# Optimization experiments

Measured on AMD Instinct MI355X. Metric: run time of the kernel, lower is better.

Reference implementation:

```python
import jax, jax.numpy as jnp
import numpy as np

T, B, S, V, D = 64, 32, 400, 32000, 1536  # timesteps, batch, post len, vocab, dh+2*eh


def setup_inputs() -> dict:
    key = jax.random.key(0)
    k0, k1, k2, k3, k4 = jax.random.split(key, 5)
    return {
        "h": jax.random.normal(k0, (T, B, D), jnp.float32),
        "W": jax.random.normal(k1, (D, V), jnp.float32) * 0.02,
        "b": jnp.zeros((V,), jnp.float32),
        # attention weights over post positions (rows sum to 1, like the model's softmax attention)
        "att": jax.nn.softmax(jax.random.normal(k2, (T, B, S), jnp.float32), axis=-1),
        # generation probability in (0,1)
        "p_gen": jax.nn.sigmoid(jax.random.normal(k3, (T, B, 1), jnp.float32)),
        # post token ids, seq-first (S, B) as in the original data layout
        "post": jax.random.randint(k4, (S, B), 0, V),
    }


def reference(h, W, b, att, p_gen, post):
    # gen.w = wLinearLayer(gen.h): (T,B,D) @ (D,V) + (V,)
    w = jnp.einsum('tbd,dv->tbv', h, W) + b
    # sum_on_voc_index: scatter-add att[t,b,s] into voc_att[t,b,post[s,b]].
    # (The torch code builds a dense (B,V,S) zero buffer, scatter_'s the same
    # positions every timestep and sums over S -- identical to this scatter-add.)
    idx = post.T                                   # (B, S)
    b_idx = jnp.arange(B)[:, None]                 # (B, 1) -> broadcasts with idx
    voc_att = jnp.zeros((T, B, V), w.dtype).at[:, b_idx, idx].add(att)
    # pointer-generator mixture
    return p_gen * w + (1.0 - p_gen) * voc_att
```

## Files before the change

### kernel.cpp

```cpp
#include <hip/hip_runtime.h>
#include <hip/hip_bf16.h>
#include <stdint.h>

#define T_DIM 64
#define B_DIM 32
#define S_DIM 400
#define V_DIM 32000
#define D_DIM 1536
#define M_DIM (T_DIM * B_DIM)

typedef __attribute__((ext_vector_type(8))) short bf16x8;
typedef __attribute__((ext_vector_type(4))) float f32x4;


static __device__ __forceinline__ unsigned short f2bf(float x) {
    union { float f; uint32_t u; } v; v.f = x;
    uint32_t r = (v.u + 0x7FFFu + ((v.u >> 16) & 1u)) >> 16;
    return (unsigned short)r;
}

static __device__ __forceinline__ void gload_lds16(const void* g, void* l) {
    __builtin_amdgcn_global_load_lds(
        (const __attribute__((address_space(1))) uint32_t*)g,
        (__attribute__((address_space(3))) uint32_t*)l,
        16, 0, 0);
}


__global__ void convert_h(const float* __restrict__ h, unsigned short* __restrict__ hb) {
    const size_t n4 = (size_t)M_DIM * D_DIM / 4;
    for (size_t i = (size_t)blockIdx.x * blockDim.x + threadIdx.x; i < n4;
         i += (size_t)gridDim.x * blockDim.x) {
        const float4 v = ((const float4*)h)[i];
        ushort4 o;
        o.x = f2bf(v.x); o.y = f2bf(v.y); o.z = f2bf(v.z); o.w = f2bf(v.w);
        ((ushort4*)hb)[i] = o;
    }
}


__global__ __launch_bounds__(256)
void convT_W(const float* __restrict__ W, unsigned short* __restrict__ Wt) {
    __shared__ unsigned short lds[64 * 66];
    const int k0 = blockIdx.x * 64;
    const int v0 = blockIdx.y * 64;
    const int tid = threadIdx.x;
    const int rr = tid >> 4;
    const int cc = (tid & 15) * 4;

    #pragma unroll
    for (int p = 0; p < 4; ++p) {
        const int r = p * 16 + rr;
        const float4 v = *(const float4*)&W[(size_t)(k0 + r) * V_DIM + v0 + cc];
        unsigned short* q = &lds[r * 66 + cc];
        q[0] = f2bf(v.x); q[1] = f2bf(v.y); q[2] = f2bf(v.z); q[3] = f2bf(v.w);
    }
    __syncthreads();
    #pragma unroll
    for (int p = 0; p < 4; ++p) {
        const int n = p * 16 + rr;
        ushort4 o;
        o.x = lds[(cc + 0) * 66 + n];
        o.y = lds[(cc + 1) * 66 + n];
        o.z = lds[(cc + 2) * 66 + n];
        o.w = lds[(cc + 3) * 66 + n];
        *(ushort4*)&Wt[(size_t)(v0 + n) * D_DIM + k0 + cc] = o;
    }
}


#define BM 128
#define BN 128
#define BK 32
#define NKT (D_DIM / BK)

__global__ __launch_bounds__(256, 2)
void gemm_mfma(const unsigned short* __restrict__ A,
               const unsigned short* __restrict__ Bt,
               const float* __restrict__ bias,
               const float* __restrict__ p_gen,
               float* __restrict__ out) {
    __shared__ unsigned short lds[2][2][BM * BK];

    const int bid = blockIdx.x;
    const int mt = bid & 15;
    const int nt = bid >> 4;
    const int m0 = mt * BM;
    const int n0 = nt * BN;
    const int tid = threadIdx.x;
    const int lane = tid & 63;
    const int wid = tid >> 6;
    const int wr = wid >> 1;
    const int wc = wid & 1;

    f32x4 acc[4][4] = {};

    auto stage = [&](int buf, int kt) {
        const int k0 = kt * BK;
        #pragma unroll
        for (int i = 0; i < 2; ++i) {
            const int o = tid * 16 + i * 4096;
            const int row = o >> 6;
            const int colb = o & 63;
            const char* ga = (const char*)A + ((size_t)(m0 + row) * D_DIM + k0) * 2 + colb;
            gload_lds16(ga, (char*)&lds[buf][0][0] + o);
            const char* gb = (const char*)Bt + ((size_t)(n0 + row) * D_DIM + k0) * 2 + colb;
            gload_lds16(gb, (char*)&lds[buf][1][0] + o);
        }
    };

    const int kq = (lane >> 4) * 8;
    const int rq = lane & 15;

    auto compute = [&](int buf) {
        const unsigned short* As = &lds[buf][0][0];
        const unsigned short* Bs = &lds[buf][1][0];
        bf16x8 a[4], b[4];
        #pragma unroll
        for (int i = 0; i < 4; ++i) {
            a[i] = *(const bf16x8*)&As[(wr * 64 + i * 16 + rq) * BK + kq];
            b[i] = *(const bf16x8*)&Bs[(wc * 64 + i * 16 + rq) * BK + kq];
        }
        #pragma unroll
        for (int mi = 0; mi < 4; ++mi)
            #pragma unroll
            for (int ni = 0; ni < 4; ++ni)
                acc[mi][ni] = __builtin_amdgcn_mfma_f32_16x16x32_bf16(a[mi], b[ni], acc[mi][ni], 0, 0, 0);
    };

    stage(0, 0);
    int cur = 0;
    for (int kt = 0; kt < NKT; ++kt) {
        __syncthreads();
        if (kt + 1 < NKT) stage(cur ^ 1, kt + 1);
        compute(cur);
        cur ^= 1;
    }

    const int rr4 = (lane >> 4) * 4;
    #pragma unroll
    for (int mi = 0; mi < 4; ++mi) {
        #pragma unroll
        for (int r = 0; r < 4; ++r) {
            const int m = m0 + wr * 64 + mi * 16 + rr4 + r;
            const float pg = p_gen[m];
            #pragma unroll
            for (int ni = 0; ni < 4; ++ni) {
                const int n = n0 + wc * 64 + ni * 16 + rq;
                out[(size_t)m * V_DIM + n] = pg * (acc[mi][ni][r] + bias[n]);
            }
        }
    }
}


__global__ void scatter_att(const float* __restrict__ att, const float* __restrict__ p_gen,
                            const int* __restrict__ post, float* __restrict__ out) {
    const int tb = blockIdx.x;
    const int b = tb & (B_DIM - 1);
    const float g = 1.0f - p_gen[tb];
    float* o = out + (size_t)tb * V_DIM;
    const float* a = att + (size_t)tb * S_DIM;
    for (int s = threadIdx.x; s < S_DIM; s += blockDim.x) {
        atomicAdd(&o[post[s * B_DIM + b]], g * a[s]);
    }
}


#define FB_MT 16
__global__ __launch_bounds__(256)
void gemm_naive(const float* __restrict__ h, const float* __restrict__ W,
                const float* __restrict__ bias, const float* __restrict__ pg,
                float* __restrict__ out) {
    const int mb = blockIdx.y;
    const int v = blockIdx.x * 256 + threadIdx.x;
    __shared__ float hs[FB_MT][128];
    float acc[FB_MT] = {};
    for (int k0 = 0; k0 < D_DIM; k0 += 128) {
        for (int i = threadIdx.x; i < FB_MT * 128; i += 256)
            hs[i >> 7][i & 127] = h[(size_t)(mb * FB_MT + (i >> 7)) * D_DIM + k0 + (i & 127)];
        __syncthreads();
        for (int kk = 0; kk < 128; ++kk) {
            const float wv = W[(size_t)(k0 + kk) * V_DIM + v];
            #pragma unroll
            for (int i = 0; i < FB_MT; ++i) acc[i] += hs[i][kk] * wv;
        }
        __syncthreads();
    }
    #pragma unroll
    for (int i = 0; i < FB_MT; ++i) {
        const int m = mb * FB_MT + i;
        out[(size_t)m * V_DIM + v] = pg[m] * (acc[i] + bias[v]);
    }
}


extern "C" void kernel_launch(void* const* d_in, const int* in_sizes, int n_in,
                              void* d_out, int out_size, void* d_ws, size_t ws_size,
                              hipStream_t stream) {
    const float* h    = (const float*)d_in[0];
    const float* W    = (const float*)d_in[1];
    const float* bias = (const float*)d_in[2];
    const float* att  = (const float*)d_in[3];
    const float* pg   = (const float*)d_in[4];
    const int*   post = (const int*)d_in[5];
    float* out = (float*)d_out;

    const size_t wt_bytes = (size_t)V_DIM * D_DIM * 2;
    const size_t hb_bytes = (size_t)M_DIM * D_DIM * 2;

    if (ws_size >= wt_bytes + hb_bytes) {
        unsigned short* Wt = (unsigned short*)d_ws;
        unsigned short* hb = (unsigned short*)((char*)d_ws + wt_bytes);
        convert_h<<<1024, 256, 0, stream>>>(h, hb);
        dim3 tg(D_DIM / 64, V_DIM / 64);
        convT_W<<<tg, 256, 0, stream>>>(W, Wt);
        gemm_mfma<<<16 * 250, 256, 0, stream>>>(hb, Wt, bias, pg, out);
    } else {
        dim3 fg(V_DIM / 256, M_DIM / FB_MT);
        gemm_naive<<<fg, 256, 0, stream>>>(h, W, bias, pg, out);
    }

    scatter_att<<<M_DIM, 256, 0, stream>>>(att, pg, post, out);
}
```

Before: 389.6 us.

## Replace 128x128 GEMM with 256x256-tile 4-stage pipelined MFMA kernel

Replaces the bf16 MFMA GEMM with a 512-thread kernel that computes 256x256 output tiles. It uses a 4-buffer LDS ring with loads issued three k-steps ahead and tracked by explicit vmcnt waits. An XOR swizzle on LDS addresses is meant to avoid bank conflicts, a block-index swizzle is meant to improve L2 reuse of W tiles, and s_setprio is raised around the MFMA bursts. The larger tiles cut global and LDS traffic per FLOP, at the cost of about 128KB of LDS per block, so residency is likely one block per CU, plus more barriers per k-step.

```diff
diff --git a/kernel.cpp b/kernel.cpp
--- a/kernel.cpp
+++ b/kernel.cpp
@@ -11,6 +11,9 @@
 
 typedef __attribute__((ext_vector_type(8))) short bf16x8;
 typedef __attribute__((ext_vector_type(4))) float f32x4;
+
+#define MEMFENCE asm volatile("" ::: "memory")
+#define BARRIER() do { MEMFENCE; __builtin_amdgcn_s_barrier(); MEMFENCE; } while (0)
 
 
 static __device__ __forceinline__ unsigned short f2bf(float x) {
@@ -69,88 +72,124 @@
 }
 
 
-#define BM 128
-#define BN 128
-#define BK 32
-#define NKT (D_DIM / BK)
-
-__global__ __launch_bounds__(256, 2)
-void gemm_mfma(const unsigned short* __restrict__ A,
-               const unsigned short* __restrict__ Bt,
-               const float* __restrict__ bias,
-               const float* __restrict__ p_gen,
-               float* __restrict__ out) {
-    __shared__ unsigned short lds[2][2][BM * BK];
+#define GBM 256
+#define GBN 256
+#define GBK 32
+#define GNKT (D_DIM / GBK)
+
+__global__ __launch_bounds__(512, 2)
+void gemm_mfma256(const unsigned short* __restrict__ A,
+                  const unsigned short* __restrict__ Bt,
+                  const float* __restrict__ bias,
+                  const float* __restrict__ p_gen,
+                  float* __restrict__ out) {
+    __shared__ unsigned short ldsA[4][GBM * GBK];
+    __shared__ unsigned short ldsB[4][GBN * GBK];
 
     const int bid = blockIdx.x;
-    const int mt = bid & 15;
-    const int nt = bid >> 4;
-    const int m0 = mt * BM;
-    const int n0 = nt * BN;
+    const int swz = (bid & 7) * 125 + (bid >> 3);
+    const int m0 = (swz & 7) * GBM;
+    const int n0 = (swz >> 3) * GBN;
+
     const int tid = threadIdx.x;
     const int lane = tid & 63;
     const int wid = tid >> 6;
-    const int wr = wid >> 1;
-    const int wc = wid & 1;
-
-    f32x4 acc[4][4] = {};
-
-    auto stage = [&](int buf, int kt) {
-        const int k0 = kt * BK;
-        #pragma unroll
-        for (int i = 0; i < 2; ++i) {
-            const int o = tid * 16 + i * 4096;
-            const int row = o >> 6;
-            const int colb = o & 63;
-            const char* ga = (const char*)A + ((size_t)(m0 + row) * D_DIM + k0) * 2 + colb;
-            gload_lds16(ga, (char*)&lds[buf][0][0] + o);
-            const char* gb = (const char*)Bt + ((size_t)(n0 + row) * D_DIM + k0) * 2 + colb;
-            gload_lds16(gb, (char*)&lds[buf][1][0] + o);
-        }
-    };
-
+    const int wr = wid >> 2;
+    const int wc = wid & 3;
+    const int rq = lane & 15;
     const int kq = (lane >> 4) * 8;
-    const int rq = lane & 15;
-
-    auto compute = [&](int buf) {
-        const unsigned short* As = &lds[buf][0][0];
-        const unsigned short* Bs = &lds[buf][1][0];
+
+    const char* gA[2]; const char* gB[2]; int ldsOff[2];
+    #pragma unroll
+    for (int j = 0; j < 2; ++j) {
+        const int o = tid * 16 + j * 8192;
+        const int row = o >> 6;
+        const int lc = (o & 63) ^ (((row >> 1) & 3) << 4);
+        gA[j] = (const char*)A + (size_t)(m0 + row) * D_DIM * 2 + lc;
+        gB[j] = (const char*)Bt + (size_t)(n0 + row) * D_DIM * 2 + lc;
+        ldsOff[j] = o;
+    }
+
+    #define STAGE2(kt, j)                                                        \
+        do {                                                                     \
+            const int _b = (kt) & 3;                                             \
+            gload_lds16(gA[j] + (size_t)(kt) * (GBK * 2),                        \
+                        (char*)&ldsA[_b][0] + ldsOff[j]);                        \
+            gload_lds16(gB[j] + (size_t)(kt) * (GBK * 2),                        \
+                        (char*)&ldsB[_b][0] + ldsOff[j]);                        \
+        } while (0)
+
+    int aOff0[4], aOff1[4], bOff[4];
+    #pragma unroll
+    for (int i = 0; i < 4; ++i) {
+        int r0 = wr * 128 + i * 16 + rq;
+        int r1 = r0 + 64;
+        aOff0[i] = r0 * 64 + ((kq * 2) ^ (((r0 >> 1) & 3) << 4));
+        aOff1[i] = r1 * 64 + ((kq * 2) ^ (((r1 >> 1) & 3) << 4));
+        int rb = wc * 64 + i * 16 + rq;
+        bOff[i] = rb * 64 + ((kq * 2) ^ (((rb >> 1) & 3) << 4));
+    }
+
+    f32x4 acc[8][4] = {};
+
+    #pragma unroll
+    for (int t = 0; t < 3; ++t) { STAGE2(t, 0); STAGE2(t, 1); }
+    asm volatile("s_waitcnt vmcnt(8)" ::: "memory");
+    BARRIER();
+
+    for (int kt = 0; kt < GNKT; ++kt) {
+        const char* As = (const char*)&ldsA[kt & 3][0];
+        const char* Bs = (const char*)&ldsB[kt & 3][0];
         bf16x8 a[4], b[4];
-        #pragma unroll
-        for (int i = 0; i < 4; ++i) {
-            a[i] = *(const bf16x8*)&As[(wr * 64 + i * 16 + rq) * BK + kq];
-            b[i] = *(const bf16x8*)&Bs[(wc * 64 + i * 16 + rq) * BK + kq];
-        }
+
+        #pragma unroll
+        for (int i = 0; i < 4; ++i) a[i] = *(const bf16x8*)(As + aOff0[i]);
+        #pragma unroll
+        for (int j = 0; j < 4; ++j) b[j] = *(const bf16x8*)(Bs + bOff[j]);
+        if (kt + 3 < GNKT) STAGE2(kt + 3, 0);
+        BARRIER();
+        __builtin_amdgcn_s_setprio(1);
         #pragma unroll
         for (int mi = 0; mi < 4; ++mi)
             #pragma unroll
-            for (int ni = 0; ni < 4; ++ni)
-                acc[mi][ni] = __builtin_amdgcn_mfma_f32_16x16x32_bf16(a[mi], b[ni], acc[mi][ni], 0, 0, 0);
-    };
-
-    stage(0, 0);
-    int cur = 0;
-    for (int kt = 0; kt < NKT; ++kt) {
-        __syncthreads();
-        if (kt + 1 < NKT) stage(cur ^ 1, kt + 1);
-        compute(cur);
-        cur ^= 1;
+            for (int nj = 0; nj < 4; ++nj)
+                acc[mi][nj] = __builtin_amdgcn_mfma_f32_16x16x32_bf16(a[mi], b[nj], acc[mi][nj], 0, 0, 0);
+        __builtin_amdgcn_s_setprio(0);
+        BARRIER();
+
+        #pragma unroll
+        for (int i = 0; i < 4; ++i) a[i] = *(const bf16x8*)(As + aOff1[i]);
+        if (kt + 3 < GNKT) STAGE2(kt + 3, 1);
+        BARRIER();
+        __builtin_amdgcn_s_setprio(1);
+        #pragma unroll
+        for (int mi = 0; mi < 4; ++mi)
+            #pragma unroll
+            for (int nj = 0; nj < 4; ++nj)
+                acc[4 + mi][nj] = __builtin_amdgcn_mfma_f32_16x16x32_bf16(a[mi], b[nj], acc[4 + mi][nj], 0, 0, 0);
+        __builtin_amdgcn_s_setprio(0);
+
+        if (kt < GNKT - 3)       { asm volatile("s_waitcnt vmcnt(8)" ::: "memory"); }
+        else if (kt == GNKT - 3) { asm volatile("s_waitcnt vmcnt(4)" ::: "memory"); }
+        else if (kt == GNKT - 2) { asm volatile("s_waitcnt vmcnt(0)" ::: "memory"); }
+        BARRIER();
     }
 
     const int rr4 = (lane >> 4) * 4;
     #pragma unroll
-    for (int mi = 0; mi < 4; ++mi) {
+    for (int mi = 0; mi < 8; ++mi) {
         #pragma unroll
         for (int r = 0; r < 4; ++r) {
-            const int m = m0 + wr * 64 + mi * 16 + rr4 + r;
-            const float pg = p_gen[m];
-            #pragma unroll
-            for (int ni = 0; ni < 4; ++ni) {
-                const int n = n0 + wc * 64 + ni * 16 + rq;
-                out[(size_t)m * V_DIM + n] = pg * (acc[mi][ni][r] + bias[n]);
+            const int m = m0 + wr * 128 + mi * 16 + rr4 + r;
+            const float pgv = p_gen[m];
+            #pragma unroll
+            for (int nj = 0; nj < 4; ++nj) {
+                const int n = n0 + wc * 64 + nj * 16 + rq;
+                out[(size_t)m * V_DIM + n] = pgv * (acc[mi][nj][r] + bias[n]);
             }
         }
     }
+    #undef STAGE2
 }
 
 
@@ -215,7 +254,7 @@
         convert_h<<<1024, 256, 0, stream>>>(h, hb);
         dim3 tg(D_DIM / 64, V_DIM / 64);
         convT_W<<<tg, 256, 0, stream>>>(W, Wt);
-        gemm_mfma<<<16 * 250, 256, 0, stream>>>(hb, Wt, bias, pg, out);
+        gemm_mfma256<<<(M_DIM / GBM) * (V_DIM / GBN), 512, 0, stream>>>(hb, Wt, bias, pg, out);
     } else {
         dim3 fg(V_DIM / 256, M_DIM / FB_MT);
         gemm_naive<<<fg, 256, 0, stream>>>(h, W, bias, pg, out);
```

Result: slower. 397.6 us (+2.1%).

## Restructure MFMA GEMM: 256x128 tiles, direct-register B loads, swizzled LDS A

Applied to the files above, without the earlier changes.

Replaces the 128x128x32 GEMM with a 256x128x64 tile in which only A is staged into LDS, using an XOR-swizzled layout to avoid bank conflicts. Each wave loads its B fragments straight from global memory into registers, one K step ahead. Block IDs are remapped so that blocks running at the same time share A/B tiles in cache, and the barrier uses a partial vmcnt wait instead of a full sync. This aims to cut LDS traffic and synchronisation overhead and raise reuse, at the cost of higher register pressure (32 accumulators plus double-buffered B) and possibly uncoalesced global B loads.

```diff
diff --git a/kernel.cpp b/kernel.cpp
--- a/kernel.cpp
+++ b/kernel.cpp
@@ -11,6 +11,9 @@
 
 typedef __attribute__((ext_vector_type(8))) short bf16x8;
 typedef __attribute__((ext_vector_type(4))) float f32x4;
+
+#define MEMFENCE asm volatile("" ::: "memory")
+#define BARRIER() do { MEMFENCE; __builtin_amdgcn_s_barrier(); MEMFENCE; } while (0)
 
 
 static __device__ __forceinline__ unsigned short f2bf(float x) {
@@ -69,85 +72,114 @@
 }
 
 
-#define BM 128
-#define BN 128
-#define BK 32
-#define NKT (D_DIM / BK)
+#define BM2 256
+#define BN2 128
+#define BK2 64
+#define NKT2 (D_DIM / BK2)
 
 __global__ __launch_bounds__(256, 2)
-void gemm_mfma(const unsigned short* __restrict__ A,
-               const unsigned short* __restrict__ Bt,
-               const float* __restrict__ bias,
-               const float* __restrict__ p_gen,
-               float* __restrict__ out) {
-    __shared__ unsigned short lds[2][2][BM * BK];
+void gemm_bdirect(const unsigned short* __restrict__ A,
+                  const unsigned short* __restrict__ Bt,
+                  const float* __restrict__ bias,
+                  const float* __restrict__ p_gen,
+                  float* __restrict__ out) {
+    __shared__ unsigned short ldsA[2][BM2 * BK2];
 
     const int bid = blockIdx.x;
-    const int mt = bid & 15;
-    const int nt = bid >> 4;
-    const int m0 = mt * BM;
-    const int n0 = nt * BN;
+    const int swz = (bid & 7) * 250 + (bid >> 3);
+    const int m0 = (swz & 7) * BM2;
+    const int n0 = (swz >> 3) * BN2;
+
     const int tid = threadIdx.x;
     const int lane = tid & 63;
     const int wid = tid >> 6;
     const int wr = wid >> 1;
     const int wc = wid & 1;
-
-    f32x4 acc[4][4] = {};
-
-    auto stage = [&](int buf, int kt) {
-        const int k0 = kt * BK;
-        #pragma unroll
-        for (int i = 0; i < 2; ++i) {
-            const int o = tid * 16 + i * 4096;
-            const int row = o >> 6;
-            const int colb = o & 63;
-            const char* ga = (const char*)A + ((size_t)(m0 + row) * D_DIM + k0) * 2 + colb;
-            gload_lds16(ga, (char*)&lds[buf][0][0] + o);
-            const char* gb = (const char*)Bt + ((size_t)(n0 + row) * D_DIM + k0) * 2 + colb;
-            gload_lds16(gb, (char*)&lds[buf][1][0] + o);
-        }
-    };
-
-    const int kq = (lane >> 4) * 8;
     const int rq = lane & 15;
-
-    auto compute = [&](int buf) {
-        const unsigned short* As = &lds[buf][0][0];
-        const unsigned short* Bs = &lds[buf][1][0];
-        bf16x8 a[4], b[4];
-        #pragma unroll
-        for (int i = 0; i < 4; ++i) {
-            a[i] = *(const bf16x8*)&As[(wr * 64 + i * 16 + rq) * BK + kq];
-            b[i] = *(const bf16x8*)&Bs[(wc * 64 + i * 16 + rq) * BK + kq];
-        }
-        #pragma unroll
-        for (int mi = 0; mi < 4; ++mi)
-            #pragma unroll
-            for (int ni = 0; ni < 4; ++ni)
-                acc[mi][ni] = __builtin_amdgcn_mfma_f32_16x16x32_bf16(a[mi], b[ni], acc[mi][ni], 0, 0, 0);
-    };
-
-    stage(0, 0);
-    int cur = 0;
-    for (int kt = 0; kt < NKT; ++kt) {
-        __syncthreads();
-        if (kt + 1 < NKT) stage(cur ^ 1, kt + 1);
-        compute(cur);
-        cur ^= 1;
+    const int kq = lane >> 4;
+
+    uint32_t gAoff[8];
+    #pragma unroll
+    for (int i = 0; i < 8; ++i) {
+        const int o = tid * 16 + i * 4096;
+        const int row = o >> 7;
+        const int col = (o & 127) ^ ((row & 7) << 4);
+        gAoff[i] = (uint32_t)((m0 + row) * (D_DIM * 2) + col);
+    }
+
+    int aOff[2][8];
+    #pragma unroll
+    for (int ks = 0; ks < 2; ++ks)
+        #pragma unroll
+        for (int mi = 0; mi < 8; ++mi) {
+            const int row = wr * 128 + mi * 16 + rq;
+            aOff[ks][mi] = row * 128 + ((ks * 64 + kq * 16) ^ ((row & 7) << 4));
+        }
+
+    const char* gB = (const char*)Bt + (size_t)(n0 + wc * 64 + rq) * (D_DIM * 2) + kq * 16;
+
+    f32x4 acc[8][4] = {};
+    bf16x8 bE[4][2], bO[4][2];
+
+    auto stageA = [&](int t) {
+        char* dst = (char*)&ldsA[t & 1][0] + tid * 16;
+        const char* base = (const char*)A + (size_t)t * (BK2 * 2);
+        #pragma unroll
+        for (int i = 0; i < 8; ++i)
+            gload_lds16(base + gAoff[i], dst + i * 4096);
+    };
+    auto bload = [&](int t, bf16x8 (&bb)[4][2]) {
+        const char* p = gB + (size_t)t * (BK2 * 2);
+        #pragma unroll
+        for (int nj = 0; nj < 4; ++nj)
+            #pragma unroll
+            for (int ks = 0; ks < 2; ++ks)
+                bb[nj][ks] = *(const bf16x8*)(p + (size_t)nj * (16 * D_DIM * 2) + ks * 64);
+    };
+    auto compute = [&](int t, bf16x8 (&bc)[4][2]) {
+        const char* As = (const char*)&ldsA[t & 1][0];
+        #pragma unroll
+        for (int ks = 0; ks < 2; ++ks) {
+            #pragma unroll
+            for (int mh = 0; mh < 2; ++mh) {
+                bf16x8 a[4];
+                #pragma unroll
+                for (int i = 0; i < 4; ++i) a[i] = *(const bf16x8*)(As + aOff[ks][mh * 4 + i]);
+                #pragma unroll
+                for (int i = 0; i < 4; ++i)
+                    #pragma unroll
+                    for (int nj = 0; nj < 4; ++nj)
+                        acc[mh * 4 + i][nj] = __builtin_amdgcn_mfma_f32_16x16x32_bf16(
+                            a[i], bc[nj][ks], acc[mh * 4 + i][nj], 0, 0, 0);
+            }
+        }
+    };
+
+    auto body = [&](int t, bf16x8 (&bc)[4][2], bf16x8 (&bn)[4][2]) {
+        asm volatile("s_waitcnt vmcnt(8)" ::: "memory");
+        BARRIER();
+        if (t + 1 < NKT2) { stageA(t + 1); bload(t + 1, bn); }
+        compute(t, bc);
+    };
+
+    stageA(0);
+    bload(0, bE);
+    for (int t = 0; t < NKT2; t += 2) {
+        body(t, bE, bO);
+        body(t + 1, bO, bE);
     }
 
     const int rr4 = (lane >> 4) * 4;
     #pragma unroll
-    for (int mi = 0; mi < 4; ++mi) {
+    for (int mi = 0; mi < 8; ++mi) {
         #pragma unroll
         for (int r = 0; r < 4; ++r) {
-            const int m = m0 + wr * 64 + mi * 16 + rr4 + r;
-            const float pg = p_gen[m];
-            #pragma unroll
-            for (int ni = 0; ni < 4; ++ni) {
-                const int n = n0 + wc * 64 + ni * 16 + rq;
-                out[(size_t)m * V_DIM + n] = pg * (acc[mi][ni][r] + bias[n]);
+            const int m = m0 + wr * 128 + mi * 16 + rr4 + r;
+            const float pgv = p_gen[m];
+            #pragma unroll
+            for (int nj = 0; nj < 4; ++nj) {
+                const int n = n0 + wc * 64 + nj * 16 + rq;
+                out[(size_t)m * V_DIM + n] = pgv * (acc[mi][nj][r] + bias[n]);
             }
         }
     }
@@ -215,7 +247,7 @@
         convert_h<<<1024, 256, 0, stream>>>(h, hb);
         dim3 tg(D_DIM / 64, V_DIM / 64);
         convT_W<<<tg, 256, 0, stream>>>(W, Wt);
-        gemm_mfma<<<16 * 250, 256, 0, stream>>>(hb, Wt, bias, pg, out);
+        gemm_bdirect<<<(M_DIM / BM2) * (V_DIM / BN2), 256, 0, stream>>>(hb, Wt, bias, pg, out);
     } else {
         dim3 fg(V_DIM / 256, M_DIM / FB_MT);
         gemm_naive<<<fg, 256, 0, stream>>>(h, W, bias, pg, out);
```

Result: slower. 525.9 us (+35.0%).

## Restructure MFMA GEMM with 256x128 tiles, triple-buffered LDS, swizzle and block remap

Applied to the files above, without the earlier changes.

Replaces the 128x128 double-buffered GEMM with a 512-thread, 256x128-tile kernel that uses a three-stage LDS ring with prefetch two iterations ahead and explicit vmcnt waits in place of full syncthreads. LDS columns are XOR-swizzled to reduce bank conflicts on the fragment reads. Block indices are remapped so that neighbouring blocks share M tiles for L2 reuse, and s_setprio is raised around the MFMA burst. This uses more LDS per block, and the hand-placed waitcnts add the risk of ordering hazards in the pipeline.

```diff
diff --git a/kernel.cpp b/kernel.cpp
--- a/kernel.cpp
+++ b/kernel.cpp
@@ -11,6 +11,9 @@
 
 typedef __attribute__((ext_vector_type(8))) short bf16x8;
 typedef __attribute__((ext_vector_type(4))) float f32x4;
+
+#define MEMFENCE asm volatile("" ::: "memory")
+#define BARRIER() do { MEMFENCE; __builtin_amdgcn_s_barrier(); MEMFENCE; } while (0)
 
 
 static __device__ __forceinline__ unsigned short f2bf(float x) {
@@ -69,72 +72,99 @@
 }
 
 
-#define BM 128
-#define BN 128
-#define BK 32
-#define NKT (D_DIM / BK)
-
-__global__ __launch_bounds__(256, 2)
-void gemm_mfma(const unsigned short* __restrict__ A,
-               const unsigned short* __restrict__ Bt,
-               const float* __restrict__ bias,
-               const float* __restrict__ p_gen,
-               float* __restrict__ out) {
-    __shared__ unsigned short lds[2][2][BM * BK];
+#define BM4 256
+#define BN4 128
+#define BK4 32
+#define NKT4 (D_DIM / BK4)
+
+__global__ __launch_bounds__(512, 4)
+void gemm_occ(const unsigned short* __restrict__ A,
+              const unsigned short* __restrict__ Bt,
+              const float* __restrict__ bias,
+              const float* __restrict__ p_gen,
+              float* __restrict__ out) {
+    __shared__ char lds[73728];
 
     const int bid = blockIdx.x;
-    const int mt = bid & 15;
-    const int nt = bid >> 4;
-    const int m0 = mt * BM;
-    const int n0 = nt * BN;
+    const int swz = (bid & 7) * 250 + (bid >> 3);
+    const int m0 = (swz & 7) * BM4;
+    const int n0 = (swz >> 3) * BN4;
+
     const int tid = threadIdx.x;
     const int lane = tid & 63;
     const int wid = tid >> 6;
     const int wr = wid >> 1;
     const int wc = wid & 1;
+    const int rq = lane & 15;
+    const int kq = lane >> 4;
+
+    const char* pA[2];
+    int stOA[2];
+    #pragma unroll
+    for (int j = 0; j < 2; ++j) {
+        const int o = tid * 16 + j * 8192;
+        const int row = o >> 6;
+        const int col = (o & 63) ^ ((row & 3) << 4);
+        pA[j] = (const char*)A + (size_t)(m0 + row) * (D_DIM * 2) + col;
+        stOA[j] = o;
+    }
+    const char* pB;
+    const int stOB = tid * 16;
+    {
+        const int row = stOB >> 6;
+        const int col = (stOB & 63) ^ ((row & 3) << 4);
+        pB = (const char*)Bt + (size_t)(n0 + row) * (D_DIM * 2) + col;
+    }
+
+    auto stage = [&](int t) {
+        char* bufA = lds + (t % 3) * 16384;
+        char* bufB = lds + 49152 + (t % 3) * 8192;
+        gload_lds16(pA[0] + t * (BK4 * 2), bufA + stOA[0]);
+        gload_lds16(pA[1] + t * (BK4 * 2), bufA + stOA[1]);
+        gload_lds16(pB + t * (BK4 * 2), bufB + stOB);
+    };
+
+    int aOff[4], bOff[4];
+    #pragma unroll
+    for (int i = 0; i < 4; ++i) {
+        const int ra = wr * 64 + i * 16 + rq;
+        aOff[i] = ra * 64 + ((kq * 16) ^ ((ra & 3) << 4));
+        const int rb = wc * 64 + i * 16 + rq;
+        bOff[i] = rb * 64 + ((kq * 16) ^ ((rb & 3) << 4));
+    }
 
     f32x4 acc[4][4] = {};
 
-    auto stage = [&](int buf, int kt) {
-        const int k0 = kt * BK;
-        #pragma unroll
-        for (int i = 0; i < 2; ++i) {
-            const int o = tid * 16 + i * 4096;
-            const int row = o >> 6;
-            const int colb = o & 63;
-            const char* ga = (const char*)A + ((size_t)(m0 + row) * D_DIM + k0) * 2 + colb;
-            gload_lds16(ga, (char*)&lds[buf][0][0] + o);
-            const char* gb = (const char*)Bt + ((size_t)(n0 + row) * D_DIM + k0) * 2 + colb;
-            gload_lds16(gb, (char*)&lds[buf][1][0] + o);
-        }
-    };
-
-    const int kq = (lane >> 4) * 8;
-    const int rq = lane & 15;
-
-    auto compute = [&](int buf) {
-        const unsigned short* As = &lds[buf][0][0];
-        const unsigned short* Bs = &lds[buf][1][0];
-        bf16x8 a[4], b[4];
-        #pragma unroll
-        for (int i = 0; i < 4; ++i) {
-            a[i] = *(const bf16x8*)&As[(wr * 64 + i * 16 + rq) * BK + kq];
-            b[i] = *(const bf16x8*)&Bs[(wc * 64 + i * 16 + rq) * BK + kq];
-        }
+    stage(0);
+    stage(1);
+    asm volatile("s_waitcnt vmcnt(3)" ::: "memory");
+    BARRIER();
+
+    #pragma unroll 3
+    for (int t = 0; t < NKT4; ++t) {
+        const char* bufA = lds + (t % 3) * 16384;
+        const char* bufB = lds + 49152 + (t % 3) * 8192;
+
+        bf16x8 aF[4], bF[4];
+        #pragma unroll
+        for (int i = 0; i < 4; ++i) aF[i] = *(const bf16x8*)(bufA + aOff[i]);
+        #pragma unroll
+        for (int i = 0; i < 4; ++i) bF[i] = *(const bf16x8*)(bufB + bOff[i]);
+
+        if (t + 2 < NKT4) stage(t + 2);
+
+        __builtin_amdgcn_s_setprio(1);
         #pragma unroll
         for (int mi = 0; mi < 4; ++mi)
             #pragma unroll
-            for (int ni = 0; ni < 4; ++ni)
-                acc[mi][ni] = __builtin_amdgcn_mfma_f32_16x16x32_bf16(a[mi], b[ni], acc[mi][ni], 0, 0, 0);
-    };
-
-    stage(0, 0);
-    int cur = 0;
-    for (int kt = 0; kt < NKT; ++kt) {
-        __syncthreads();
-        if (kt + 1 < NKT) stage(cur ^ 1, kt + 1);
-        compute(cur);
-        cur ^= 1;
+            for (int nj = 0; nj < 4; ++nj)
+                acc[mi][nj] = __builtin_amdgcn_mfma_f32_16x16x32_bf16(
+                    aF[mi], bF[nj], acc[mi][nj], 0, 0, 0);
+        __builtin_amdgcn_s_setprio(0);
+
+        if (t + 2 < NKT4)      { asm volatile("s_waitcnt vmcnt(3)" ::: "memory"); }
+        else if (t + 1 < NKT4) { asm volatile("s_waitcnt vmcnt(0)" ::: "memory"); }
+        if (t + 1 < NKT4) BARRIER();
     }
 
     const int rr4 = (lane >> 4) * 4;
@@ -143,11 +173,11 @@
         #pragma unroll
         for (int r = 0; r < 4; ++r) {
             const int m = m0 + wr * 64 + mi * 16 + rr4 + r;
-            const float pg = p_gen[m];
+            const float pgv = p_gen[m];
             #pragma unroll
-            for (int ni = 0; ni < 4; ++ni) {
-                const int n = n0 + wc * 64 + ni * 16 + rq;
-                out[(size_t)m * V_DIM + n] = pg * (acc[mi][ni][r] + bias[n]);
+            for (int nj = 0; nj < 4; ++nj) {
+                const int n = n0 + wc * 64 + nj * 16 + rq;
+                out[(size_t)m * V_DIM + n] = pgv * (acc[mi][nj][r] + bias[n]);
             }
         }
     }
@@ -215,7 +245,7 @@
         convert_h<<<1024, 256, 0, stream>>>(h, hb);
         dim3 tg(D_DIM / 64, V_DIM / 64);
         convT_W<<<tg, 256, 0, stream>>>(W, Wt);
-        gemm_mfma<<<16 * 250, 256, 0, stream>>>(hb, Wt, bias, pg, out);
+        gemm_occ<<<(M_DIM / BM4) * (V_DIM / BN4), 512, 0, stream>>>(hb, Wt, bias, pg, out);
     } else {
         dim3 fg(V_DIM / 256, M_DIM / FB_MT);
         gemm_naive<<<fg, 256, 0, stream>>>(h, W, bias, pg, out);
```

Measured after the change: 561.0 us. 44.0% more time.
